# Performance work log

Measured on AMD Instinct MI355X. Metric: run time of the kernel, lower is better.

The kernel has to match this reference:

```python
import jax, jax.numpy as jnp
import numpy as np

IN_CH, EMBED_DIM, N_CODES = 8, 64, 512


def conv1d(x, w, b, stride, pad):
    # x: [B,C,T], w: [O,I,K] (torch Conv1d layout)
    y = jax.lax.conv_general_dilated(x, w, (stride,), [(pad, pad)],
                                     dimension_numbers=('NCH', 'OIH', 'NCH'))
    return y + b[None, :, None]


def conv_transpose1d(x, w, b, stride, pad):
    # w: [I,O,K] (torch ConvTranspose1d layout); equiv to lhs-dilated conv with flipped kernel
    k = w.shape[2]
    wf = jnp.flip(jnp.transpose(w, (1, 0, 2)), axis=2)  # [O,I,K]
    y = jax.lax.conv_general_dilated(x, wf, (1,), [(k - 1 - pad, k - 1 - pad)],
                                     lhs_dilation=(stride,),
                                     dimension_numbers=('NCH', 'OIH', 'NCH'))
    return y + b[None, :, None]


def setup_inputs() -> dict:
    key = jax.random.key(0)
    ks = jax.random.split(key, 16)
    def p(k, shape, fan_in):
        lim = 1.0 / np.sqrt(fan_in)
        return jax.random.uniform(k, shape, jnp.float32, -lim, lim)
    x = jax.random.normal(ks[0], (16, IN_CH, 32768), jnp.float32)
    # encoder convs (torch Conv1d: [out,in,k])
    w1 = p(ks[1], (64, IN_CH, 7), IN_CH * 7);   b1 = p(ks[2], (64,), IN_CH * 7)
    w2 = p(ks[3], (128, 64, 5), 64 * 5);        b2 = p(ks[4], (128,), 64 * 5)
    w3 = p(ks[5], (EMBED_DIM, 128, 3), 128 * 3); b3 = p(ks[6], (EMBED_DIM,), 128 * 3)
    codebook = jax.random.uniform(ks[7], (N_CODES, EMBED_DIM), jnp.float32,
                                  -1.0 / N_CODES, 1.0 / N_CODES)
    # decoder conv-transposes (torch ConvTranspose1d: [in,out,k])
    dw1 = p(ks[8], (EMBED_DIM, 128, 4), EMBED_DIM * 4); db1 = p(ks[9], (128,), EMBED_DIM * 4)
    dw2 = p(ks[10], (128, 64, 4), 128 * 4);             db2 = p(ks[11], (64,), 128 * 4)
    dw3 = p(ks[12], (64, IN_CH, 4), 64 * 4);            db3 = p(ks[13], (IN_CH,), 64 * 4)
    return {'x': x, 'w1': w1, 'b1': b1, 'w2': w2, 'b2': b2, 'w3': w3, 'b3': b3,
            'codebook': codebook, 'dw1': dw1, 'db1': db1, 'dw2': dw2, 'db2': db2,
            'dw3': dw3, 'db3': db3}


def quantize(z_e, codebook):
    # z_e: [B,D,T]
    B, D, T = z_e.shape
    z_flat = jnp.transpose(z_e, (0, 2, 1)).reshape(-1, D)  # [B*T, D]
    # squared euclidean distances [B*T, n_codes]
    d2 = (jnp.sum(z_flat * z_flat, axis=1, keepdims=True)
          - 2.0 * z_flat @ codebook.T
          + jnp.sum(codebook * codebook, axis=1)[None, :])
    indices = jnp.argmin(d2, axis=1)
    z_q = codebook[indices].reshape(B, T, D).transpose(0, 2, 1)  # [B,D,T]
    return z_q, indices.reshape(B, T)


def mse(a, b):
    d = a - b
    return jnp.mean(d * d)


def reference(x, w1, b1, w2, b2, w3, b3, codebook, dw1, db1, dw2, db2, dw3, db3):
    sg = jax.lax.stop_gradient
    z = jax.nn.relu(conv1d(x, w1, b1, 2, 3))
    z = jax.nn.relu(conv1d(z, w2, b2, 2, 2))
    z_e = conv1d(z, w3, b3, 2, 1)  # [B, D, T/8]
    z_q, indices = quantize(z_e, codebook)
    z_q_st = z_e + sg(z_q - z_e)  # straight-through
    r = jax.nn.relu(conv_transpose1d(z_q_st, dw1, db1, 2, 1))
    r = jax.nn.relu(conv_transpose1d(r, dw2, db2, 2, 1))
    x_recon = conv_transpose1d(r, dw3, db3, 2, 1)  # [B, C, T]
    vq_loss = mse(sg(z_q), z_e)
    commitment_loss = mse(sg(z_e), z_q)
    T = min(x.shape[-1], x_recon.shape[-1])
    recon_loss = mse(x_recon[..., :T], x[..., :T])
    conditioning = jnp.mean(z_q_st, axis=-1)  # [B, D]
    return conditioning, vq_loss, commitment_loss, recon_loss
```

## Files before the change

### kernel.cpp

```cpp
#include <hip/hip_runtime.h>
#include <hip/hip_bf16.h>


#define NB 16
#define T0 32768
#define T1 16384
#define T2 8192
#define T3 4096
#define NCODES 512
#define EDIM 64

typedef __attribute__((ext_vector_type(8)))  short short8;
typedef __attribute__((ext_vector_type(16))) float f32x16;
typedef __attribute__((ext_vector_type(16))) unsigned u32x16;
typedef __attribute__((ext_vector_type(4)))  float f32x4;

__device__ __forceinline__ float b2f(short s) {
    unsigned u = ((unsigned)(unsigned short)s) << 16;
    float f; __builtin_memcpy(&f, &u, 4); return f;
}
__device__ __forceinline__ short f2bs(float f) {
    __hip_bfloat16 h = __float2bfloat16(f);
    short s; __builtin_memcpy(&s, &h, 2); return s;
}
__device__ __forceinline__ unsigned f2ord(float s) {
    unsigned u = __float_as_uint(s);
    return u ^ ((unsigned)((int)u >> 31) | 0x80000000u);
}

__device__ __forceinline__ float block_sum256(float v) {
    #pragma unroll
    for (int off = 32; off > 0; off >>= 1) v += __shfl_down(v, off, 64);
    __shared__ float red[4];
    int lane = threadIdx.x & 63, wv = threadIdx.x >> 6;
    if (lane == 0) red[wv] = v;
    __syncthreads();
    return red[0] + red[1] + red[2] + red[3];
}

__global__ __launch_bounds__(256, 2)
void conv1_mfma(const float* __restrict__ x, const short* __restrict__ w1b,
                const float* __restrict__ b1, short* __restrict__ y) {
    constexpr int BT = 128, NR = 262;
    __shared__ short lxc[NR * 8];
    __shared__ short lw[64 * 64];
    int tid = threadIdx.x, b = blockIdx.z, t0 = blockIdx.x * BT;
    for (int i = tid; i < 512; i += 256) {
        int oc = i >> 3, c8 = i & 7;
        short8 v = *(const short8*)(w1b + oc * 64 + c8 * 8);
        *(short8*)(lw + oc * 64 + (c8 ^ (oc & 7)) * 8) = v;
    }
    for (int r = tid; r < NR; r += 256) {
        int g = 2 * t0 - 3 + r;
        short8 p;
        bool ok = (unsigned)g < (unsigned)T0;
        #pragma unroll
        for (int ic = 0; ic < 8; ic++) {
            float v = ok ? x[((size_t)b * 8 + ic) * T0 + g] : 0.f;
            p[ic] = f2bs(v);
        }
        *(short8*)(lxc + r * 8) = p;
    }
    __syncthreads();
    int wv = tid >> 6, lane = tid & 63, lm = lane & 31, lk = lane >> 5;
    int ml = wv * 32 + lm;
    f32x16 acc[2];
    #pragma unroll
    for (int oj = 0; oj < 2; oj++)
        #pragma unroll
        for (int r = 0; r < 16; r++) acc[oj][r] = 0.f;
    #pragma unroll
    for (int kc = 0; kc < 4; kc++) {
        int q = kc * 2 + lk;
        short8 a = *(const short8*)(lxc + (2 * ml + q) * 8);
        #pragma unroll
        for (int oj = 0; oj < 2; oj++) {
            int oc = oj * 32 + lm;
            short8 bf = *(const short8*)(lw + oc * 64 + (q ^ (oc & 7)) * 8);
            acc[oj] = __builtin_amdgcn_mfma_f32_32x32x16_bf16(a, bf, acc[oj], 0, 0, 0);
        }
    }
    #pragma unroll
    for (int oj = 0; oj < 2; oj++) {
        int oc = oj * 32 + lm;
        float bs = b1[oc];
        #pragma unroll
        for (int r = 0; r < 16; r++) {
            int t = t0 + wv * 32 + (r & 3) + 8 * (r >> 2) + 4 * lk;
            float v = fmaxf(acc[oj][r] + bs, 0.f);
            y[((size_t)b * T1 + t) * 64 + oc] = f2bs(v);
        }
    }
}

template<int IC, int OC, int OCB, int TAPS, int PAD, int BT, int NW, bool RELU, bool F32OUT>
__global__ __launch_bounds__(NW * 64, 2)
void conv_mfma_fwd(const short* __restrict__ x, const short* __restrict__ wb,
                   const float* __restrict__ bias, void* __restrict__ yout,
                   int Tin, int Tout) {
    constexpr int C8 = IC / 8;
    constexpr int NR = 2 * (BT - 1) + TAPS;
    __shared__ short lw[TAPS * OCB * IC];
    __shared__ short lx[NR * IC];
    const int tid = threadIdx.x;
    const int b   = blockIdx.z;
    const int ocg = blockIdx.y * OCB;
    const int t0  = blockIdx.x * BT;
    const int r0  = 2 * t0 - PAD;
    for (int i = tid; i < TAPS * OCB * C8; i += NW * 64) {
        int tap = i / (OCB * C8), rem = i - tap * OCB * C8;
        int ocl = rem / C8, c8 = rem - ocl * C8;
        short8 v = *(const short8*)(wb + ((size_t)tap * OC + ocg + ocl) * IC + c8 * 8);
        *(short8*)(lw + (tap * OCB + ocl) * IC + (c8 ^ (ocl & (C8 - 1))) * 8) = v;
    }
    const short* xg = x + (size_t)b * Tin * IC;
    short8 zz = {0, 0, 0, 0, 0, 0, 0, 0};
    for (int idx = tid; idx < NR * C8; idx += NW * 64) {
        int row = idx / C8, c8 = idx - row * C8;
        int gr = r0 + row;
        short8 v = zz;
        if ((unsigned)gr < (unsigned)Tin)
            v = *(const short8*)(xg + (size_t)gr * IC + c8 * 8);
        *(short8*)(lx + row * IC + (c8 ^ ((row >> 1) & (C8 - 1))) * 8) = v;
    }
    __syncthreads();

    const int wv = tid >> 6, lane = tid & 63;
    const int tl = wv * 32;
    const int lm = lane & 31, lk = lane >> 5;
    f32x16 acc[OCB / 32];
    #pragma unroll
    for (int oj = 0; oj < OCB / 32; oj++)
        #pragma unroll
        for (int r = 0; r < 16; r++) acc[oj][r] = 0.f;

    #pragma unroll
    for (int tap = 0; tap < TAPS; tap++) {
        #pragma unroll
        for (int kc = 0; kc < IC / 16; kc++) {
            int row = 2 * (tl + lm) + tap;
            int c8  = kc * 2 + lk;
            short8 a = *(const short8*)(lx + row * IC + (c8 ^ ((row >> 1) & (C8 - 1))) * 8);
            #pragma unroll
            for (int oj = 0; oj < OCB / 32; oj++) {
                int ocl = oj * 32 + lm;
                short8 bf = *(const short8*)(lw + (tap * OCB + ocl) * IC +
                                             (c8 ^ (ocl & (C8 - 1))) * 8);
                acc[oj] = __builtin_amdgcn_mfma_f32_32x32x16_bf16(a, bf, acc[oj], 0, 0, 0);
            }
        }
    }
    #pragma unroll
    for (int oj = 0; oj < OCB / 32; oj++) {
        int oc = ocg + oj * 32 + lm;
        float bs = bias[oc];
        #pragma unroll
        for (int r = 0; r < 16; r++) {
            int t = t0 + tl + (r & 3) + 8 * (r >> 2) + 4 * lk;
            float v = acc[oj][r] + bs;
            if (RELU) v = fmaxf(v, 0.f);
            if (F32OUT)
                ((float*)yout)[((size_t)b * Tout + t) * OC + oc] = v;
            else
                ((short*)yout)[((size_t)b * Tout + t) * OC + oc] = f2bs(v);
        }
    }
}

template<int IC, int OC, int OCB, int BT, int NW, bool RELU>
__global__ __launch_bounds__(NW * 64, 2)
void conv_mfma_t(const short* __restrict__ x, const short* __restrict__ wb,
                 const float* __restrict__ bias, short* __restrict__ y, int Tin) {
    constexpr int C8 = IC / 8;
    constexpr int NR = BT + 2;
    __shared__ short lw[4 * OCB * IC];
    __shared__ short lx[NR * IC];
    const int tid = threadIdx.x;
    const int b   = blockIdx.z;
    const int ocg = blockIdx.y * OCB;
    const int m0  = blockIdx.x * BT;
    const int r0  = m0 - 1;
    for (int i = tid; i < 4 * OCB * C8; i += NW * 64) {
        int k = i / (OCB * C8), rem = i - k * OCB * C8;
        int ocl = rem / C8, c8 = rem - ocl * C8;
        short8 v = *(const short8*)(wb + ((size_t)k * OC + ocg + ocl) * IC + c8 * 8);
        *(short8*)(lw + (k * OCB + ocl) * IC + (c8 ^ (ocl & (C8 - 1))) * 8) = v;
    }
    const short* xg = x + (size_t)b * Tin * IC;
    short8 zz = {0, 0, 0, 0, 0, 0, 0, 0};
    for (int idx = tid; idx < NR * C8; idx += NW * 64) {
        int row = idx / C8, c8 = idx - row * C8;
        int gr = r0 + row;
        short8 v = zz;
        if ((unsigned)gr < (unsigned)Tin)
            v = *(const short8*)(xg + (size_t)gr * IC + c8 * 8);
        *(short8*)(lx + row * IC + (c8 ^ ((row >> 1) & (C8 - 1))) * 8) = v;
    }
    __syncthreads();

    const int wv = tid >> 6, lane = tid & 63;
    const int ml = wv * 32;
    const int lm = lane & 31, lk = lane >> 5;
    f32x16 accE[OCB / 32], accO[OCB / 32];
    #pragma unroll
    for (int oj = 0; oj < OCB / 32; oj++)
        #pragma unroll
        for (int r = 0; r < 16; r++) { accE[oj][r] = 0.f; accO[oj][r] = 0.f; }

    #pragma unroll
    for (int kc = 0; kc < IC / 16; kc++) {
        int c8 = kc * 2 + lk;
        int rA = ml + lm;
        short8 a_m1, a_0, a_p1;
        {
            int row = rA;
            a_m1 = *(const short8*)(lx + row * IC + (c8 ^ ((row >> 1) & (C8 - 1))) * 8);
            row = rA + 1;
            a_0  = *(const short8*)(lx + row * IC + (c8 ^ ((row >> 1) & (C8 - 1))) * 8);
            row = rA + 2;
            a_p1 = *(const short8*)(lx + row * IC + (c8 ^ ((row >> 1) & (C8 - 1))) * 8);
        }
        #pragma unroll
        for (int oj = 0; oj < OCB / 32; oj++) {
            int ocl = oj * 32 + lm;
            int sw = (c8 ^ (ocl & (C8 - 1))) * 8;
            short8 w0 = *(const short8*)(lw + ((0 * OCB + ocl) * IC) + sw);
            short8 w1 = *(const short8*)(lw + ((1 * OCB + ocl) * IC) + sw);
            short8 w2 = *(const short8*)(lw + ((2 * OCB + ocl) * IC) + sw);
            short8 w3 = *(const short8*)(lw + ((3 * OCB + ocl) * IC) + sw);
            accE[oj] = __builtin_amdgcn_mfma_f32_32x32x16_bf16(a_0,  w1, accE[oj], 0, 0, 0);
            accE[oj] = __builtin_amdgcn_mfma_f32_32x32x16_bf16(a_m1, w3, accE[oj], 0, 0, 0);
            accO[oj] = __builtin_amdgcn_mfma_f32_32x32x16_bf16(a_p1, w0, accO[oj], 0, 0, 0);
            accO[oj] = __builtin_amdgcn_mfma_f32_32x32x16_bf16(a_0,  w2, accO[oj], 0, 0, 0);
        }
    }
    int Tout = 2 * Tin;
    #pragma unroll
    for (int oj = 0; oj < OCB / 32; oj++) {
        int oc = ocg + oj * 32 + lm;
        float bs = bias[oc];
        #pragma unroll
        for (int r = 0; r < 16; r++) {
            int m = m0 + ml + (r & 3) + 8 * (r >> 2) + 4 * lk;
            float ve = accE[oj][r] + bs;
            float vo = accO[oj][r] + bs;
            if (RELU) { ve = fmaxf(ve, 0.f); vo = fmaxf(vo, 0.f); }
            short* yp = y + ((size_t)b * Tout + 2 * m) * OC + oc;
            yp[0]  = f2bs(ve);
            yp[OC] = f2bs(vo);
        }
    }
}

__global__ __launch_bounds__(256, 2)
void convt3_loss(const short* __restrict__ r2, const short* __restrict__ w3m,
                 const float* __restrict__ db3, const float* __restrict__ x,
                 float* __restrict__ acc) {
    constexpr int BT = 256, NR = 258;
    __shared__ short lr[NR * 64];
    __shared__ short lw[16 * 200];
    __shared__ float lxt[8 * 512];
    int tid = threadIdx.x, b = blockIdx.z, m0 = blockIdx.x * BT;
    for (int i = tid; i < 384; i += 256) {
        int n = i / 24, kc = i - n * 24;
        *(short8*)(lw + n * 200 + kc * 8) = *(const short8*)(w3m + n * 192 + kc * 8);
    }
    const short* rb = r2 + (size_t)b * T1 * 64;
    short8 zz = {0, 0, 0, 0, 0, 0, 0, 0};
    for (int i = tid; i < NR * 8; i += 256) {
        int r = i >> 3, c8 = i & 7;
        int g = m0 - 1 + r;
        short8 v = zz;
        if ((unsigned)g < (unsigned)T1)
            v = *(const short8*)(rb + (size_t)g * 64 + c8 * 8);
        *(short8*)(lr + r * 64 + (c8 ^ (r & 7)) * 8) = v;
    }
    const float* xb = x + (size_t)b * 8 * T0;
    for (int i = tid; i < 1024; i += 256) {
        int oc = i >> 7, c4 = (i & 127) * 4;
        *(float4*)(lxt + oc * 512 + c4) =
            *(const float4*)(xb + (size_t)oc * T0 + 2 * m0 + c4);
    }
    __syncthreads();
    int wv = tid >> 6, lane = tid & 63;
    int row16 = lane & 15, quad = lane >> 4;
    short8 bfr[6];
    #pragma unroll
    for (int kb = 0; kb < 6; kb++)
        bfr[kb] = *(const short8*)(lw + row16 * 200 + kb * 32 + quad * 8);
    f32x4 accv[4];
    #pragma unroll
    for (int rg = 0; rg < 4; rg++) accv[rg] = (f32x4){0.f, 0.f, 0.f, 0.f};
    #pragma unroll
    for (int kb = 0; kb < 6; kb++) {
        int kg = kb * 32 + quad * 8;
        int ro = kg >> 6, c8 = (kg >> 3) & 7;
        #pragma unroll
        for (int rg = 0; rg < 4; rg++) {
            int r = wv * 64 + rg * 16 + row16 + ro;
            short8 a = *(const short8*)(lr + r * 64 + (c8 ^ (r & 7)) * 8);
            accv[rg] = __builtin_amdgcn_mfma_f32_16x16x32_bf16(a, bfr[kb], accv[rg], 0, 0, 0);
        }
    }
    int oc = row16 & 7, par = row16 >> 3;
    float bs = db3[oc];
    float s = 0.f;
    #pragma unroll
    for (int rg = 0; rg < 4; rg++)
        #pragma unroll
        for (int reg = 0; reg < 4; reg++) {
            int ml = wv * 64 + rg * 16 + quad * 4 + reg;
            float v = accv[rg][reg] + bs;
            float d = v - lxt[oc * 512 + 2 * ml + par];
            s += d * d;
        }
    s = block_sum256(s);
    if (tid == 0) atomicAdd(acc + 1, s);
}

__global__ void prep_kernel(const float* __restrict__ cb, const float* __restrict__ w1,
                            const float* __restrict__ w2, const float* __restrict__ w3,
                            const float* __restrict__ dw1, const float* __restrict__ dw2,
                            const float* __restrict__ dw3,
                            float* __restrict__ c2, float* __restrict__ cond,
                            float* __restrict__ acc,
                            short* __restrict__ wb2, short* __restrict__ wb3,
                            short* __restrict__ wT1, short* __restrict__ wT2,
                            short* __restrict__ cbbf, short* __restrict__ w1b,
                            short* __restrict__ w3m) {
    int i = blockIdx.x * 256 + threadIdx.x;
    if (i < 8) acc[i] = 0.f;
    if (i < 1024) cond[i] = 0.f;
    if (i < NCODES) {
        float s = 0.f;
        #pragma unroll
        for (int d = 0; d < EDIM; d++) { float v = cb[i * EDIM + d]; s += v * v; }
        c2[i] = s;
    }
    if (i < 32768) cbbf[i] = f2bs(cb[i]);
    if (i < 4096) {
        int oc = i >> 6, k = i & 63;
        int ic = k & 7, q = k >> 3;
        w1b[i] = (q < 7) ? f2bs(w1[((size_t)oc * 8 + ic) * 7 + q]) : (short)0;
    }
    if (i < 3072) {
        int n = i / 192, k = i - (i / 192) * 192;
        int oc = n & 7;
        float v = 0.f;
        if (n < 8) {
            if (k < 64)       v = dw3[((size_t)k * 8 + oc) * 4 + 3];
            else if (k < 128) v = dw3[((size_t)(k - 64) * 8 + oc) * 4 + 1];
        } else {
            if (k >= 128)     v = dw3[((size_t)(k - 128) * 8 + oc) * 4 + 0];
            else if (k >= 64) v = dw3[((size_t)(k - 64) * 8 + oc) * 4 + 2];
        }
        w3m[i] = f2bs(v);
    }
    if (i < 40960) {
        int tap = i / 8192, r = i - tap * 8192;
        int oc = r >> 6, ic = r & 63;
        wb2[i] = f2bs(w2[((size_t)oc * 64 + ic) * 5 + tap]);
    }
    if (i < 24576) {
        int tap = i / 8192, r = i - tap * 8192;
        int oc = r >> 7, ic = r & 127;
        wb3[i] = f2bs(w3[((size_t)oc * 128 + ic) * 3 + tap]);
    }
    if (i < 32768) {
        int k = i / 8192, r = i - k * 8192;
        int oc = r >> 6, ic = r & 63;
        wT1[i] = f2bs(dw1[((size_t)ic * 128 + oc) * 4 + k]);
    }
    if (i < 32768) {
        int k = i / 8192, r = i - k * 8192;
        int oc = r >> 7, ic = r & 127;
        wT2[i] = f2bs(dw2[((size_t)ic * 64 + oc) * 4 + k]);
    }
}

__global__ __launch_bounds__(256, 2)
void conv3_quant(const short* __restrict__ a2, const short* __restrict__ wb3,
                 const float* __restrict__ b3, const float* __restrict__ cb,
                 const short* __restrict__ cbbf, const float* __restrict__ c2g,
                 short* __restrict__ zq, float* __restrict__ cond,
                 float* __restrict__ accg) {
    constexpr int IC = 128, C8 = IC / 8;
    constexpr int BT = 128;
    constexpr int NR = 2 * (BT - 1) + 3;
    __shared__ short lx[NR * IC];
    __shared__ float lc2[NCODES];
    __shared__ int   ibuf[BT];
    __shared__ float scr[4 * 64];
    int tid = threadIdx.x, b = blockIdx.z, t0 = blockIdx.x * BT;
    int r0 = 2 * t0 - 1;
    for (int i = tid; i < NCODES; i += 256) lc2[i] = c2g[i];
    const short* xg = a2 + (size_t)b * T2 * IC;
    short8 zz = {0, 0, 0, 0, 0, 0, 0, 0};
    for (int idx = tid; idx < NR * C8; idx += 256) {
        int row = idx >> 4, c8 = idx & 15;
        int gr = r0 + row;
        short8 v = zz;
        if ((unsigned)gr < (unsigned)T2)
            v = *(const short8*)(xg + (size_t)gr * IC + c8 * 8);
        *(short8*)(lx + row * IC + (c8 ^ ((row >> 1) & 15)) * 8) = v;
    }
    __syncthreads();

    int wv = tid >> 6, lane = tid & 63, lm = lane & 31, lk = lane >> 5;
    int tl = wv * 32;
    f32x16 acc[2];
    #pragma unroll
    for (int oj = 0; oj < 2; oj++)
        #pragma unroll
        for (int r = 0; r < 16; r++) acc[oj][r] = 0.f;
    #pragma unroll
    for (int tap = 0; tap < 3; tap++) {
        #pragma unroll
        for (int kc = 0; kc < 8; kc++) {
            int row = 2 * (tl + lm) + tap;
            int c8  = kc * 2 + lk;
            short8 a = *(const short8*)(lx + row * IC + (c8 ^ ((row >> 1) & 15)) * 8);
            #pragma unroll
            for (int oj = 0; oj < 2; oj++) {
                short8 bf = *(const short8*)(wb3 +
                    ((size_t)tap * 64 + oj * 32 + lm) * IC + c8 * 8);
                acc[oj] = __builtin_amdgcn_mfma_f32_32x32x16_bf16(a, bf, acc[oj], 0, 0, 0);
            }
        }
    }
    float bs0 = b3[lm], bs1 = b3[32 + lm];
    #pragma unroll
    for (int r = 0; r < 16; r++) { acc[0][r] += bs0; acc[1][r] += bs1; }
    __syncthreads();

    short* lzq = lx;
    #pragma unroll
    for (int oj = 0; oj < 2; oj++) {
        int oc = oj * 32 + lm;
        #pragma unroll
        for (int r = 0; r < 16; r++) {
            int tloc = tl + (r & 3) + 8 * (r >> 2) + 4 * lk;
            lzq[tloc * 64 + (((oc >> 3) ^ (tloc & 7)) * 8) + (oc & 7)] = f2bs(acc[oj][r]);
        }
    }
    __syncthreads();

    int arow = wv * 32 + lm;
    short8 afr[4];
    #pragma unroll
    for (int kc = 0; kc < 4; kc++) {
        int c8 = kc * 2 + lk;
        afr[kc] = *(const short8*)(lzq + arow * 64 + ((c8 ^ (arow & 7)) * 8));
    }
    u32x16 bestp;
    #pragma unroll
    for (int r = 0; r < 16; r++) bestp[r] = 0xFFFFFFFFu;
    for (int ct = 0; ct < 16; ct++) {
        f32x16 aq;
        #pragma unroll
        for (int r = 0; r < 16; r++) aq[r] = 0.f;
        const short* wg = cbbf + ((size_t)(ct * 32 + lm)) * 64 + lk * 8;
        #pragma unroll
        for (int kc = 0; kc < 4; kc++) {
            short8 bf = *(const short8*)(wg + kc * 16);
            aq = __builtin_amdgcn_mfma_f32_32x32x16_bf16(afr[kc], bf, aq, 0, 0, 0);
        }
        unsigned cidx = (unsigned)(ct * 32 + lm);
        float c2v = lc2[cidx];
        #pragma unroll
        for (int r = 0; r < 16; r++) {
            float s = c2v - 2.f * aq[r];
            unsigned p = (f2ord(s) & 0xFFFFFE00u) | cidx;
            bestp[r] = (p < bestp[r]) ? p : bestp[r];
        }
    }
    #pragma unroll
    for (int r = 0; r < 16; r++) {
        unsigned p = bestp[r];
        #pragma unroll
        for (int mk = 1; mk < 32; mk <<= 1) {
            unsigned op = (unsigned)__shfl_xor((int)p, mk, 64);
            p = (op < p) ? op : p;
        }
        if (lm == 0) ibuf[wv * 32 + (r & 3) + 8 * (r >> 2) + 4 * lk] = (int)(p & 511u);
    }
    __syncthreads();

    float vql = 0.f, cpart0 = 0.f, cpart1 = 0.f;
    short* zqb = zq + ((size_t)(b * T3 + t0)) * 64;
    #pragma unroll
    for (int r = 0; r < 16; r++) {
        int tloc = tl + (r & 3) + 8 * (r >> 2) + 4 * lk;
        int code = ibuf[tloc];
        const float* cv = cb + (size_t)code * 64;
        float c0 = cv[lm], c1 = cv[32 + lm];
        float d0 = acc[0][r] - c0, d1 = acc[1][r] - c1;
        vql += d0 * d0 + d1 * d1;
        cpart0 += c0; cpart1 += c1;
        zqb[(size_t)tloc * 64 + lm]      = f2bs(c0);
        zqb[(size_t)tloc * 64 + 32 + lm] = f2bs(c1);
    }
    cpart0 += __shfl_down(cpart0, 32, 64);
    cpart1 += __shfl_down(cpart1, 32, 64);
    if (lk == 0) { scr[wv * 64 + lm] = cpart0; scr[wv * 64 + 32 + lm] = cpart1; }
    __syncthreads();
    if (tid < 64) {
        float s = scr[tid] + scr[64 + tid] + scr[128 + tid] + scr[192 + tid];
        atomicAdd(cond + b * 64 + tid, s);
    }
    vql = block_sum256(vql);
    if (tid == 0) atomicAdd(accg, vql);
}

__global__ void fin_kernel(const float* __restrict__ cond,
                           const float* __restrict__ acc, float* __restrict__ out) {
    int i = threadIdx.x;
    out[i] = cond[i] * (1.f / (float)T3);
    if (i == 0) {
        float vq = acc[0] * (1.f / 4194304.f);
        out[1024] = vq;
        out[1025] = vq;
        out[1026] = acc[1] * (1.f / 4194304.f);
    }
}

extern "C" void kernel_launch(void* const* d_in, const int* in_sizes, int n_in,
                              void* d_out, int out_size, void* d_ws, size_t ws_size,
                              hipStream_t stream) {
    const float* x   = (const float*)d_in[0];
    const float* w1  = (const float*)d_in[1];
    const float* b1  = (const float*)d_in[2];
    const float* w2  = (const float*)d_in[3];
    const float* b2  = (const float*)d_in[4];
    const float* w3  = (const float*)d_in[5];
    const float* b3  = (const float*)d_in[6];
    const float* cb  = (const float*)d_in[7];
    const float* dw1 = (const float*)d_in[8];
    const float* db1 = (const float*)d_in[9];
    const float* dw2 = (const float*)d_in[10];
    const float* db2 = (const float*)d_in[11];
    const float* dw3 = (const float*)d_in[12];
    const float* db3 = (const float*)d_in[13];
    float* out = (float*)d_out;

    char* ws = (char*)d_ws;
    short* a1   = (short*)(ws);
    short* a2   = (short*)(ws + 33554432);
    short* zq   = (short*)(ws + 83886080);
    short* wb2  = (short*)(ws + 92274688);
    short* wb3  = (short*)(ws + 92356608);
    short* wT1  = (short*)(ws + 92405760);
    short* wT2  = (short*)(ws + 92471296);
    short* cbbf = (short*)(ws + 92536832);
    short* w1b  = (short*)(ws + 92602368);
    short* w3m  = (short*)(ws + 92610560);
    float* c2   = (float*)(ws + 92616704);
    float* cnd  = (float*)(ws + 92618752);
    float* acc  = (float*)(ws + 92622848);

    prep_kernel<<<160, 256, 0, stream>>>(cb, w1, w2, w3, dw1, dw2, dw3, c2, cnd,
                                         acc, wb2, wb3, wT1, wT2, cbbf, w1b, w3m);
    conv1_mfma<<<dim3(T1 / 128, 1, NB), 256, 0, stream>>>(x, w1b, b1, a1);
    conv_mfma_fwd<64, 128, 64, 5, 2, 128, 4, true, false>
        <<<dim3(T2 / 128, 2, NB), 256, 0, stream>>>(a1, wb2, b2, a2, T1, T2);
    conv3_quant<<<dim3(T3 / 128, 1, NB), 256, 0, stream>>>(a2, wb3, b3, cb, cbbf,
                                                           c2, zq, cnd, acc);
    conv_mfma_t<64, 128, 64, 128, 4, true>
        <<<dim3(T3 / 128, 2, NB), 256, 0, stream>>>(zq, wT1, db1, a2, T3);
    conv_mfma_t<128, 64, 32, 128, 4, true>
        <<<dim3(T2 / 128, 2, NB), 256, 0, stream>>>(a2, wT2, db2, a1, T2);
    convt3_loss<<<dim3(T1 / 256, 1, NB), 256, 0, stream>>>(a1, w3m, db3, x, acc);
    fin_kernel<<<1, 1024, 0, stream>>>(cnd, acc, out);
}
```

Measured before the change: 248.1 us.

## Shrink conv3_quant to single-wave blocks and drop shared-memory reductions

conv3_quant now runs one 64-thread wave per block over 32 time steps instead of four waves over 128, giving four times as many blocks. The per-block LDS buffers for codebook norms, chosen indices and partial sums go away. Codebook norms are held in registers, code indices stay in registers after the shuffle reduction, and block-wide syncs and reductions are replaced by wave shuffles plus direct atomics. The VQ-loss atomics are spread over four extra accumulator slots to reduce contention. In exchange there are more global atomics on the conditioning sums, less weight reuse per block, and a dependence on acc[2..5] being zeroed beforehand.

New measurement: 268.6 us. +8.2%, slower.

```diff
diff --git a/kernel.cpp b/kernel.cpp
--- a/kernel.cpp
+++ b/kernel.cpp
@@ -378,25 +378,25 @@
     }
 }
 
-__global__ __launch_bounds__(256, 2)
+__global__ __launch_bounds__(64, 2)
 void conv3_quant(const short* __restrict__ a2, const short* __restrict__ wb3,
                  const float* __restrict__ b3, const float* __restrict__ cb,
                  const short* __restrict__ cbbf, const float* __restrict__ c2g,
                  short* __restrict__ zq, float* __restrict__ cond,
                  float* __restrict__ accg) {
-    constexpr int IC = 128, C8 = IC / 8;
-    constexpr int BT = 128;
+    constexpr int IC = 128;
+    constexpr int BT = 32;
     constexpr int NR = 2 * (BT - 1) + 3;
     __shared__ short lx[NR * IC];
-    __shared__ float lc2[NCODES];
-    __shared__ int   ibuf[BT];
-    __shared__ float scr[4 * 64];
     int tid = threadIdx.x, b = blockIdx.z, t0 = blockIdx.x * BT;
     int r0 = 2 * t0 - 1;
-    for (int i = tid; i < NCODES; i += 256) lc2[i] = c2g[i];
+    int lm = tid & 31, lk = tid >> 5;
+    float c2r[16];
+    #pragma unroll
+    for (int ct = 0; ct < 16; ct++) c2r[ct] = c2g[ct * 32 + lm];
     const short* xg = a2 + (size_t)b * T2 * IC;
     short8 zz = {0, 0, 0, 0, 0, 0, 0, 0};
-    for (int idx = tid; idx < NR * C8; idx += 256) {
+    for (int idx = tid; idx < NR * 16; idx += 64) {
         int row = idx >> 4, c8 = idx & 15;
         int gr = r0 + row;
         short8 v = zz;
@@ -406,8 +406,6 @@
     }
     __syncthreads();
 
-    int wv = tid >> 6, lane = tid & 63, lm = lane & 31, lk = lane >> 5;
-    int tl = wv * 32;
     f32x16 acc[2];
     #pragma unroll
     for (int oj = 0; oj < 2; oj++)
@@ -417,7 +415,7 @@
     for (int tap = 0; tap < 3; tap++) {
         #pragma unroll
         for (int kc = 0; kc < 8; kc++) {
-            int row = 2 * (tl + lm) + tap;
+            int row = 2 * lm + tap;
             int c8  = kc * 2 + lk;
             short8 a = *(const short8*)(lx + row * IC + (c8 ^ ((row >> 1) & 15)) * 8);
             #pragma unroll
@@ -439,18 +437,17 @@
         int oc = oj * 32 + lm;
         #pragma unroll
         for (int r = 0; r < 16; r++) {
-            int tloc = tl + (r & 3) + 8 * (r >> 2) + 4 * lk;
+            int tloc = (r & 3) + 8 * (r >> 2) + 4 * lk;
             lzq[tloc * 64 + (((oc >> 3) ^ (tloc & 7)) * 8) + (oc & 7)] = f2bs(acc[oj][r]);
         }
     }
     __syncthreads();
 
-    int arow = wv * 32 + lm;
     short8 afr[4];
     #pragma unroll
     for (int kc = 0; kc < 4; kc++) {
         int c8 = kc * 2 + lk;
-        afr[kc] = *(const short8*)(lzq + arow * 64 + ((c8 ^ (arow & 7)) * 8));
+        afr[kc] = *(const short8*)(lzq + lm * 64 + ((c8 ^ (lm & 7)) * 8));
     }
     u32x16 bestp;
     #pragma unroll
@@ -466,7 +463,7 @@
             aq = __builtin_amdgcn_mfma_f32_32x32x16_bf16(afr[kc], bf, aq, 0, 0, 0);
         }
         unsigned cidx = (unsigned)(ct * 32 + lm);
-        float c2v = lc2[cidx];
+        float c2v = c2r[ct];
         #pragma unroll
         for (int r = 0; r < 16; r++) {
             float s = c2v - 2.f * aq[r];
@@ -474,6 +471,7 @@
             bestp[r] = (p < bestp[r]) ? p : bestp[r];
         }
     }
+    unsigned codes[16];
     #pragma unroll
     for (int r = 0; r < 16; r++) {
         unsigned p = bestp[r];
@@ -482,17 +480,15 @@
             unsigned op = (unsigned)__shfl_xor((int)p, mk, 64);
             p = (op < p) ? op : p;
         }
-        if (lm == 0) ibuf[wv * 32 + (r & 3) + 8 * (r >> 2) + 4 * lk] = (int)(p & 511u);
-    }
-    __syncthreads();
+        codes[r] = p & 511u;
+    }
 
     float vql = 0.f, cpart0 = 0.f, cpart1 = 0.f;
     short* zqb = zq + ((size_t)(b * T3 + t0)) * 64;
     #pragma unroll
     for (int r = 0; r < 16; r++) {
-        int tloc = tl + (r & 3) + 8 * (r >> 2) + 4 * lk;
-        int code = ibuf[tloc];
-        const float* cv = cb + (size_t)code * 64;
+        int tloc = (r & 3) + 8 * (r >> 2) + 4 * lk;
+        const float* cv = cb + (size_t)codes[r] * 64;
         float c0 = cv[lm], c1 = cv[32 + lm];
         float d0 = acc[0][r] - c0, d1 = acc[1][r] - c1;
         vql += d0 * d0 + d1 * d1;
@@ -502,14 +498,13 @@
     }
     cpart0 += __shfl_down(cpart0, 32, 64);
     cpart1 += __shfl_down(cpart1, 32, 64);
-    if (lk == 0) { scr[wv * 64 + lm] = cpart0; scr[wv * 64 + 32 + lm] = cpart1; }
-    __syncthreads();
-    if (tid < 64) {
-        float s = scr[tid] + scr[64 + tid] + scr[128 + tid] + scr[192 + tid];
-        atomicAdd(cond + b * 64 + tid, s);
-    }
-    vql = block_sum256(vql);
-    if (tid == 0) atomicAdd(accg, vql);
+    if (lk == 0) {
+        atomicAdd(cond + b * 64 + lm, cpart0);
+        atomicAdd(cond + b * 64 + 32 + lm, cpart1);
+    }
+    #pragma unroll
+    for (int off = 32; off > 0; off >>= 1) vql += __shfl_down(vql, off, 64);
+    if (tid == 0) atomicAdd(accg + 2 + ((blockIdx.x ^ blockIdx.z) & 3), vql);
 }
 
 __global__ void fin_kernel(const float* __restrict__ cond,
@@ -517,7 +512,7 @@
     int i = threadIdx.x;
     out[i] = cond[i] * (1.f / (float)T3);
     if (i == 0) {
-        float vq = acc[0] * (1.f / 4194304.f);
+        float vq = (acc[0] + acc[2] + acc[3] + acc[4] + acc[5]) * (1.f / 4194304.f);
         out[1024] = vq;
         out[1025] = vq;
         out[1026] = acc[1] * (1.f / 4194304.f);
@@ -563,8 +558,8 @@
     conv1_mfma<<<dim3(T1 / 128, 1, NB), 256, 0, stream>>>(x, w1b, b1, a1);
     conv_mfma_fwd<64, 128, 64, 5, 2, 128, 4, true, false>
         <<<dim3(T2 / 128, 2, NB), 256, 0, stream>>>(a1, wb2, b2, a2, T1, T2);
-    conv3_quant<<<dim3(T3 / 128, 1, NB), 256, 0, stream>>>(a2, wb3, b3, cb, cbbf,
-                                                           c2, zq, cnd, acc);
+    conv3_quant<<<dim3(T3 / 32, 1, NB), 64, 0, stream>>>(a2, wb3, b3, cb, cbbf,
+                                                         c2, zq, cnd, acc);
     conv_mfma_t<64, 128, 64, 128, 4, true>
         <<<dim3(T3 / 128, 2, NB), 256, 0, stream>>>(zq, wT1, db1, a2, T3);
     conv_mfma_t<128, 64, 32, 128, 4, true>
```

## Read conv weights straight from global memory and cover all output channels per block

Applied to the files above, without the earlier changes.

Conv2 and the second transposed conv get dedicated kernels that no longer stage weights in shared memory. Each MFMA weight fragment is read directly from global memory, which is cache-resident because the weights are small, and each block now computes all output channels. The input tile is therefore loaded once per time tile instead of once per channel group. This cuts shared-memory traffic, LDS footprint and duplicate input loads, at the cost of more accumulator registers and repeated global or L2 weight reads per wave.

After: 272.3 us (median of 2 runs). +9.8%, slower.

```diff
diff --git a/kernel.cpp b/kernel.cpp
--- a/kernel.cpp
+++ b/kernel.cpp
@@ -93,76 +93,127 @@
     }
 }
 
-template<int IC, int OC, int OCB, int TAPS, int PAD, int BT, int NW, bool RELU, bool F32OUT>
-__global__ __launch_bounds__(NW * 64, 2)
-void conv_mfma_fwd(const short* __restrict__ x, const short* __restrict__ wb,
-                   const float* __restrict__ bias, void* __restrict__ yout,
-                   int Tin, int Tout) {
+__global__ __launch_bounds__(256, 2)
+void conv2_gw(const short* __restrict__ a1, const short* __restrict__ wb2,
+              const float* __restrict__ b2, short* __restrict__ y) {
+    constexpr int IC = 64, OC = 128, TAPS = 5, PAD = 2, BT = 128;
     constexpr int C8 = IC / 8;
     constexpr int NR = 2 * (BT - 1) + TAPS;
-    __shared__ short lw[TAPS * OCB * IC];
     __shared__ short lx[NR * IC];
-    const int tid = threadIdx.x;
-    const int b   = blockIdx.z;
-    const int ocg = blockIdx.y * OCB;
-    const int t0  = blockIdx.x * BT;
-    const int r0  = 2 * t0 - PAD;
-    for (int i = tid; i < TAPS * OCB * C8; i += NW * 64) {
-        int tap = i / (OCB * C8), rem = i - tap * OCB * C8;
-        int ocl = rem / C8, c8 = rem - ocl * C8;
-        short8 v = *(const short8*)(wb + ((size_t)tap * OC + ocg + ocl) * IC + c8 * 8);
-        *(short8*)(lw + (tap * OCB + ocl) * IC + (c8 ^ (ocl & (C8 - 1))) * 8) = v;
-    }
-    const short* xg = x + (size_t)b * Tin * IC;
+    int tid = threadIdx.x, b = blockIdx.z, t0 = blockIdx.x * BT;
+    int r0 = 2 * t0 - PAD;
+    const short* xg = a1 + (size_t)b * T1 * IC;
     short8 zz = {0, 0, 0, 0, 0, 0, 0, 0};
-    for (int idx = tid; idx < NR * C8; idx += NW * 64) {
-        int row = idx / C8, c8 = idx - row * C8;
+    for (int idx = tid; idx < NR * C8; idx += 256) {
+        int row = idx >> 3, c8 = idx & 7;
         int gr = r0 + row;
         short8 v = zz;
-        if ((unsigned)gr < (unsigned)Tin)
+        if ((unsigned)gr < (unsigned)T1)
             v = *(const short8*)(xg + (size_t)gr * IC + c8 * 8);
-        *(short8*)(lx + row * IC + (c8 ^ ((row >> 1) & (C8 - 1))) * 8) = v;
-    }
-    __syncthreads();
-
-    const int wv = tid >> 6, lane = tid & 63;
-    const int tl = wv * 32;
-    const int lm = lane & 31, lk = lane >> 5;
-    f32x16 acc[OCB / 32];
-    #pragma unroll
-    for (int oj = 0; oj < OCB / 32; oj++)
+        *(short8*)(lx + row * IC + (c8 ^ ((row >> 1) & 7)) * 8) = v;
+    }
+    __syncthreads();
+    int wv = tid >> 6, lane = tid & 63, lm = lane & 31, lk = lane >> 5;
+    int tl = wv * 32;
+    f32x16 acc[4];
+    #pragma unroll
+    for (int oj = 0; oj < 4; oj++)
         #pragma unroll
         for (int r = 0; r < 16; r++) acc[oj][r] = 0.f;
-
     #pragma unroll
     for (int tap = 0; tap < TAPS; tap++) {
         #pragma unroll
         for (int kc = 0; kc < IC / 16; kc++) {
             int row = 2 * (tl + lm) + tap;
             int c8  = kc * 2 + lk;
-            short8 a = *(const short8*)(lx + row * IC + (c8 ^ ((row >> 1) & (C8 - 1))) * 8);
+            short8 a = *(const short8*)(lx + row * IC + (c8 ^ ((row >> 1) & 7)) * 8);
             #pragma unroll
-            for (int oj = 0; oj < OCB / 32; oj++) {
+            for (int oj = 0; oj < 4; oj++) {
                 int ocl = oj * 32 + lm;
-                short8 bf = *(const short8*)(lw + (tap * OCB + ocl) * IC +
-                                             (c8 ^ (ocl & (C8 - 1))) * 8);
+                short8 bf = *(const short8*)(wb2 + ((size_t)tap * OC + ocl) * IC + c8 * 8);
                 acc[oj] = __builtin_amdgcn_mfma_f32_32x32x16_bf16(a, bf, acc[oj], 0, 0, 0);
             }
         }
     }
     #pragma unroll
-    for (int oj = 0; oj < OCB / 32; oj++) {
-        int oc = ocg + oj * 32 + lm;
-        float bs = bias[oc];
+    for (int oj = 0; oj < 4; oj++) {
+        int oc = oj * 32 + lm;
+        float bs = b2[oc];
         #pragma unroll
         for (int r = 0; r < 16; r++) {
             int t = t0 + tl + (r & 3) + 8 * (r >> 2) + 4 * lk;
-            float v = acc[oj][r] + bs;
-            if (RELU) v = fmaxf(v, 0.f);
-            if (F32OUT)
-                ((float*)yout)[((size_t)b * Tout + t) * OC + oc] = v;
-            else
-                ((short*)yout)[((size_t)b * Tout + t) * OC + oc] = f2bs(v);
+            float v = fmaxf(acc[oj][r] + bs, 0.f);
+            y[((size_t)b * T2 + t) * OC + oc] = f2bs(v);
+        }
+    }
+}
+
+__global__ __launch_bounds__(256, 2)
+void convt2_gw(const short* __restrict__ x, const short* __restrict__ wT2,
+               const float* __restrict__ db2, short* __restrict__ y) {
+    constexpr int IC = 128, OC = 64, BT = 128;
+    constexpr int C8 = IC / 8;
+    constexpr int NR = BT + 2;
+    __shared__ short lx[NR * IC];
+    int tid = threadIdx.x, b = blockIdx.z, m0 = blockIdx.x * BT;
+    int r0 = m0 - 1;
+    const short* xg = x + (size_t)b * T2 * IC;
+    short8 zz = {0, 0, 0, 0, 0, 0, 0, 0};
+    for (int idx = tid; idx < NR * C8; idx += 256) {
+        int row = idx >> 4, c8 = idx & 15;
+        int gr = r0 + row;
+        short8 v = zz;
+        if ((unsigned)gr < (unsigned)T2)
+            v = *(const short8*)(xg + (size_t)gr * IC + c8 * 8);
+        *(short8*)(lx + row * IC + (c8 ^ ((row >> 1) & 15)) * 8) = v;
+    }
+    __syncthreads();
+    int wv = tid >> 6, lane = tid & 63, lm = lane & 31, lk = lane >> 5;
+    int ml = wv * 32;
+    f32x16 accE[2], accO[2];
+    #pragma unroll
+    for (int oj = 0; oj < 2; oj++)
+        #pragma unroll
+        for (int r = 0; r < 16; r++) { accE[oj][r] = 0.f; accO[oj][r] = 0.f; }
+    #pragma unroll
+    for (int kc = 0; kc < 8; kc++) {
+        int c8 = kc * 2 + lk;
+        int rA = ml + lm;
+        short8 a_m1, a_0, a_p1;
+        {
+            int row = rA;
+            a_m1 = *(const short8*)(lx + row * IC + (c8 ^ ((row >> 1) & 15)) * 8);
+            row = rA + 1;
+            a_0  = *(const short8*)(lx + row * IC + (c8 ^ ((row >> 1) & 15)) * 8);
+            row = rA + 2;
+            a_p1 = *(const short8*)(lx + row * IC + (c8 ^ ((row >> 1) & 15)) * 8);
+        }
+        #pragma unroll
+        for (int oj = 0; oj < 2; oj++) {
+            int ocl = oj * 32 + lm;
+            const short* wp = wT2 + (size_t)ocl * IC + c8 * 8;
+            short8 w0 = *(const short8*)(wp + 0 * OC * IC);
+            short8 w1 = *(const short8*)(wp + 1 * OC * IC);
+            short8 w2 = *(const short8*)(wp + 2 * OC * IC);
+            short8 w3 = *(const short8*)(wp + 3 * OC * IC);
+            accE[oj] = __builtin_amdgcn_mfma_f32_32x32x16_bf16(a_0,  w1, accE[oj], 0, 0, 0);
+            accE[oj] = __builtin_amdgcn_mfma_f32_32x32x16_bf16(a_m1, w3, accE[oj], 0, 0, 0);
+            accO[oj] = __builtin_amdgcn_mfma_f32_32x32x16_bf16(a_p1, w0, accO[oj], 0, 0, 0);
+            accO[oj] = __builtin_amdgcn_mfma_f32_32x32x16_bf16(a_0,  w2, accO[oj], 0, 0, 0);
+        }
+    }
+    #pragma unroll
+    for (int oj = 0; oj < 2; oj++) {
+        int oc = oj * 32 + lm;
+        float bs = db2[oc];
+        #pragma unroll
+        for (int r = 0; r < 16; r++) {
+            int m = m0 + ml + (r & 3) + 8 * (r >> 2) + 4 * lk;
+            float ve = fmaxf(accE[oj][r] + bs, 0.f);
+            float vo = fmaxf(accO[oj][r] + bs, 0.f);
+            short* yp = y + ((size_t)b * T1 + 2 * m) * OC + oc;
+            yp[0]  = f2bs(ve);
+            yp[OC] = f2bs(vo);
         }
     }
 }
@@ -561,14 +612,12 @@
     prep_kernel<<<160, 256, 0, stream>>>(cb, w1, w2, w3, dw1, dw2, dw3, c2, cnd,
                                          acc, wb2, wb3, wT1, wT2, cbbf, w1b, w3m);
     conv1_mfma<<<dim3(T1 / 128, 1, NB), 256, 0, stream>>>(x, w1b, b1, a1);
-    conv_mfma_fwd<64, 128, 64, 5, 2, 128, 4, true, false>
-        <<<dim3(T2 / 128, 2, NB), 256, 0, stream>>>(a1, wb2, b2, a2, T1, T2);
+    conv2_gw<<<dim3(T2 / 128, 1, NB), 256, 0, stream>>>(a1, wb2, b2, a2);
     conv3_quant<<<dim3(T3 / 128, 1, NB), 256, 0, stream>>>(a2, wb3, b3, cb, cbbf,
                                                            c2, zq, cnd, acc);
     conv_mfma_t<64, 128, 64, 128, 4, true>
         <<<dim3(T3 / 128, 2, NB), 256, 0, stream>>>(zq, wT1, db1, a2, T3);
-    conv_mfma_t<128, 64, 32, 128, 4, true>
-        <<<dim3(T2 / 128, 2, NB), 256, 0, stream>>>(a2, wT2, db2, a1, T2);
+    convt2_gw<<<dim3(T2 / 128, 1, NB), 256, 0, stream>>>(a2, wT2, db2, a1);
     convt3_loss<<<dim3(T1 / 256, 1, NB), 256, 0, stream>>>(a1, w3m, db3, x, acc);
     fin_kernel<<<1, 1024, 0, stream>>>(cnd, acc, out);
 }
```
